# Optimization experiments

Hardware: AMD Instinct MI355X
Metric: run time of the kernel (lower is better)

## Reference

```python
import jax, jax.numpy as jnp
import numpy as np

N_NODES = 100000
N_EDGES = 3200000
# (out_dim, in_dim) for the 4 BayesianLinear layers: mlp1 = [5->16, 16->32], mlp2 = [35->16, 16->1]
LAYER_DIMS = [(16, 5), (32, 16), (16, 35), (1, 16)]


def setup_inputs() -> dict:
    key = jax.random.key(0)
    ks = iter(jax.random.split(key, 32))
    inp = {}
    inp["x"] = jax.random.normal(next(ks), (N_NODES, 3), jnp.float32)
    inp["edge_attr"] = jax.random.normal(next(ks), (N_EDGES, 2), jnp.float32)
    inp["edge_index"] = jax.random.randint(next(ks), (2, N_EDGES), 0, N_NODES, dtype=jnp.int64)
    for li, (o, i) in enumerate(LAYER_DIMS, 1):
        inp[f"l{li}_wmu"] = jax.random.normal(next(ks), (o, i), jnp.float32) * 0.1
        inp[f"l{li}_wrho"] = jax.random.normal(next(ks), (o, i), jnp.float32) * 0.1 - 5.0
        inp[f"l{li}_bmu"] = jax.random.normal(next(ks), (o,), jnp.float32) * 0.1
        inp[f"l{li}_brho"] = jax.random.normal(next(ks), (o,), jnp.float32) * 0.1 - 5.0
        inp[f"l{li}_eps_w"] = jax.random.normal(next(ks), (o, i), jnp.float32)
        inp[f"l{li}_eps_b"] = jax.random.normal(next(ks), (o,), jnp.float32)
    return inp


def _bayes_linear(h, wmu, wrho, bmu, brho, eps_w, eps_b):
    # sampled weight: W = mu + softplus(rho) * eps  (blitz BayesianLinear)
    W = wmu + jax.nn.softplus(wrho) * eps_w          # [out, in]
    b = bmu + jax.nn.softplus(brho) * eps_b          # [out]
    return h @ W.T + b


def _igconv(x, edge_index, edge_attr, p1, p2, p3, p4):
    src, dst = edge_index[0], edge_index[1]          # x_j = x[src], aggregate at dst
    x_j = x[src]                                     # [E, 3] irregular gather
    m = jnp.concatenate([x_j, edge_attr], axis=1)    # [E, 5]
    m = jax.nn.relu(_bayes_linear(m, *p1))           # [E, 16]
    m = jax.nn.relu(_bayes_linear(m, *p2))           # [E, 32]
    agg = jax.ops.segment_max(m, dst, num_segments=x.shape[0])  # [N, 32]
    agg = jnp.where(jnp.isneginf(agg), 0.0, agg)     # nodes with no in-edges -> 0
    h = jnp.concatenate([x, agg], axis=1)            # [N, 35]
    h = jax.nn.relu(_bayes_linear(h, *p3))           # [N, 16]
    comb = jax.nn.sigmoid(_bayes_linear(h, *p4))     # [N, 1]
    return jnp.concatenate([x[:, :2], comb], axis=1) # [N, 3]


def reference(x, edge_attr, edge_index,
              l1_wmu, l1_wrho, l1_bmu, l1_brho, l1_eps_w, l1_eps_b,
              l2_wmu, l2_wrho, l2_bmu, l2_brho, l2_eps_w, l2_eps_b,
              l3_wmu, l3_wrho, l3_bmu, l3_brho, l3_eps_w, l3_eps_b,
              l4_wmu, l4_wrho, l4_bmu, l4_brho, l4_eps_w, l4_eps_b):
    p1 = (l1_wmu, l1_wrho, l1_bmu, l1_brho, l1_eps_w, l1_eps_b)
    p2 = (l2_wmu, l2_wrho, l2_bmu, l2_brho, l2_eps_w, l2_eps_b)
    p3 = (l3_wmu, l3_wrho, l3_bmu, l3_brho, l3_eps_w, l3_eps_b)
    p4 = (l4_wmu, l4_wrho, l4_bmu, l4_brho, l4_eps_w, l4_eps_b)
    h = x
    for _ in range(3):  # three stacked applications of the same IGConv
        h = _igconv(h, edge_index, edge_attr, p1, p2, p3, p4)
    return h
```

## Files before the change

kernel.cpp:

```cpp
#include <hip/hip_runtime.h>
#include <math.h>

#define WTOT  1233
#define PKOFS 1280
#define PKTOT 352

typedef __fp16 h2 __attribute__((ext_vector_type(2)));
typedef __fp16 f16x8 __attribute__((ext_vector_type(8)));
typedef float f32x4 __attribute__((ext_vector_type(4)));

struct ERec { int s; int d; unsigned int ea; };

__device__ __forceinline__ h2 u2h(unsigned int u) { return __builtin_bit_cast(h2, u); }
__device__ __forceinline__ unsigned int h2u(h2 h) { return __builtin_bit_cast(unsigned int, h); }
__device__ __forceinline__ unsigned int umax2(unsigned int a, unsigned int b) {
  return h2u(__builtin_elementwise_max(u2h(a), u2h(b)));
}
#define DOT2(a, b, c) __builtin_amdgcn_fdot2((a), (b), (c), false)

__device__ __forceinline__ float softplus_f(float x) {
  return fmaxf(x, 0.f) + log1pf(expf(-fabsf(x)));
}

struct PrepArgs {
  const float* wmu[4]; const float* wrho[4]; const float* epsw[4];
  const float* bmu[4]; const float* brho[4]; const float* epsb[4];
  float* out;
};

__global__ void prep_all_kernel(PrepArgs a) {
  const int wsz[4] = {80, 512, 560, 16};
  const int wof[4] = {0, 96, 640, 1216};
  const int bsz[4] = {16, 32, 16, 1};
  const int bof[4] = {80, 608, 1200, 1232};
  float* wg = a.out;
  int tid = threadIdx.x;
#pragma unroll
  for (int l = 0; l < 4; l++) {
    for (int i = tid; i < wsz[l]; i += 1024)
      wg[wof[l] + i] = a.wmu[l][i] + softplus_f(a.wrho[l][i]) * a.epsw[l][i];
    for (int i = tid; i < bsz[l]; i += 1024)
      wg[bof[l] + i] = a.bmu[l][i] + softplus_f(a.brho[l][i]) * a.epsb[l][i];
  }
  __syncthreads();
  unsigned int* wp = (unsigned int*)(wg + PKOFS);
  int t = tid;
  if (t < 16) {
    wp[t]      = h2u(h2{(__fp16)wg[t * 5 + 0], (__fp16)wg[t * 5 + 1]});
    wp[16 + t] = h2u(h2{(__fp16)wg[t * 5 + 2], (__fp16)0.f});
    wp[32 + t] = h2u(h2{(__fp16)wg[t * 5 + 3], (__fp16)wg[t * 5 + 4]});
    ((float*)wp)[304 + t] = wg[80 + t];
  }
  if (t < 32) {
    ((float*)wp)[320 + t] = wg[608 + t];
    for (int j = 0; j < 8; j++)
      wp[48 + t * 8 + j] =
          h2u(h2{(__fp16)wg[96 + t * 16 + 2 * j], (__fp16)wg[96 + t * 16 + 2 * j + 1]});
  }
}

__global__ void zero_kernel(int* __restrict__ p, int n) {
  int i = blockIdx.x * blockDim.x + threadIdx.x;
  if (i < n) p[i] = 0;
}

__global__ __launch_bounds__(1024) void bhist_kernel(const int* __restrict__ dst,
                                                     int* __restrict__ bucketCur,
                                                     int E, int NBUCK) {
  __shared__ int h[1024];
  int tid = threadIdx.x;
  for (int i = tid; i < NBUCK; i += 1024) h[i] = 0;
  __syncthreads();
  int base = blockIdx.x * 8192;
#pragma unroll
  for (int r = 0; r < 8; r++) {
    int e = base + r * 1024 + tid;
    if (e < E) atomicAdd(&h[dst[e] >> 7], 1);
  }
  __syncthreads();
  for (int i = tid; i < NBUCK; i += 1024) {
    int c = h[i];
    if (c) atomicAdd(&bucketCur[i], c);
  }
}

__global__ __launch_bounds__(1024) void scanBk_kernel(int* __restrict__ bucketCur,
                                                      int* __restrict__ bucketOff,
                                                      int NBUCK) {
  __shared__ int wsum[16];
  __shared__ int woff[16];
  int tid = threadIdx.x, lane = tid & 63, wid = tid >> 6;
  int v = (tid < NBUCK) ? bucketCur[tid] : 0;
  int x = v;
#pragma unroll
  for (int off = 1; off < 64; off <<= 1) {
    int t = __shfl_up(x, off, 64);
    if (lane >= off) x += t;
  }
  if (lane == 63) wsum[wid] = x;
  __syncthreads();
  if (wid == 0) {
    int s = (lane < 16) ? wsum[lane] : 0;
#pragma unroll
    for (int off = 1; off < 16; off <<= 1) {
      int t = __shfl_up(s, off, 64);
      if (lane >= off) s += t;
    }
    if (lane < 16) woff[lane] = s - wsum[lane];
  }
  __syncthreads();
  int excl = woff[wid] + x - v;
  if (tid < NBUCK) {
    bucketOff[tid] = excl;
    bucketCur[tid] = excl;
    if (tid == NBUCK - 1) bucketOff[NBUCK] = excl + v;
  }
}

__global__ __launch_bounds__(1024) void part_kernel(
    const int* __restrict__ src, const int* __restrict__ dst,
    const float2* __restrict__ ea, int* __restrict__ bucketCur,
    ERec* __restrict__ brec, int E, int NBUCK) {
  __shared__ int h[1024];
  int tid = threadIdx.x;
  for (int i = tid; i < NBUCK; i += 1024) h[i] = 0;
  __syncthreads();
  int base = blockIdx.x * 8192;
  int d[8], s[8];
  unsigned int a[8];
  bool v[8];
#pragma unroll
  for (int j = 0; j < 8; j++) {
    int e = base + j * 1024 + tid;
    v[j] = e < E;
    if (v[j]) {
      d[j] = dst[e];
      s[j] = src[e];
      float2 t = ea[e];
      a[j] = h2u(__builtin_amdgcn_cvt_pkrtz(t.x, t.y));
      atomicAdd(&h[d[j] >> 7], 1);
    }
  }
  __syncthreads();
  for (int i = tid; i < NBUCK; i += 1024) {
    int c = h[i];
    h[i] = c ? atomicAdd(&bucketCur[i], c) : 0;
  }
  __syncthreads();
#pragma unroll
  for (int j = 0; j < 8; j++) {
    if (v[j]) {
      int pos = atomicAdd(&h[d[j] >> 7], 1);
      ERec t; t.s = s[j]; t.d = d[j]; t.ea = a[j];
      brec[pos] = t;
    }
  }
}

__global__ __launch_bounds__(256) void deg_kernel(const ERec* __restrict__ brec,
                                                  const int* __restrict__ bucketOff,
                                                  int* __restrict__ deg, int N) {
  __shared__ int cnt[128];
  int b = blockIdx.x, tid = threadIdx.x;
  if (tid < 128) cnt[tid] = 0;
  __syncthreads();
  int e0 = bucketOff[b], e1 = bucketOff[b + 1];
  for (int i = e0 + tid; i < e1; i += 256) atomicAdd(&cnt[brec[i].d & 127], 1);
  __syncthreads();
  int node = b * 128 + tid;
  if (tid < 128 && node < N) deg[node] = cnt[tid];
}

__global__ void scanA_kernel(const int* __restrict__ deg, int* __restrict__ part, int n) {
  __shared__ int ws[16];
  int tid = threadIdx.x;
  int i = blockIdx.x * 1024 + tid;
  int v = 0;
  if (i < n) v = (deg[i] + 3) & ~3;
#pragma unroll
  for (int off = 32; off >= 1; off >>= 1) v += __shfl_down(v, off, 64);
  if ((tid & 63) == 0) ws[tid >> 6] = v;
  __syncthreads();
  if (tid == 0) {
    int s = 0;
#pragma unroll
    for (int k = 0; k < 16; k++) s += ws[k];
    part[blockIdx.x] = s;
  }
}

__global__ void scanB_kernel(int* __restrict__ part, int P, int* __restrict__ etot) {
  int lane = threadIdx.x;
  int carry = 0;
  for (int base = 0; base < P; base += 64) {
    int i = base + lane;
    int v = (i < P) ? part[i] : 0;
    int x = v;
#pragma unroll
    for (int off = 1; off < 64; off <<= 1) {
      int t = __shfl_up(x, off, 64);
      if (lane >= off) x += t;
    }
    if (i < P) part[i] = carry + x - v;
    carry += __shfl(x, 63, 64);
  }
  if (lane == 0) *etot = carry;
}

__global__ void scanC_kernel(const int* __restrict__ deg, const int* __restrict__ part,
                             int* __restrict__ cursor, int n) {
  __shared__ int wsum[16];
  __shared__ int woff[16];
  int tid = threadIdx.x, lane = tid & 63, wid = tid >> 6;
  int i = blockIdx.x * 1024 + tid;
  int v = 0;
  if (i < n) v = (deg[i] + 3) & ~3;
  int x = v;
#pragma unroll
  for (int off = 1; off < 64; off <<= 1) {
    int t = __shfl_up(x, off, 64);
    if (lane >= off) x += t;
  }
  if (lane == 63) wsum[wid] = x;
  __syncthreads();
  if (wid == 0) {
    int s = (lane < 16) ? wsum[lane] : 0;
#pragma unroll
    for (int off = 1; off < 16; off <<= 1) {
      int t = __shfl_up(s, off, 64);
      if (lane >= off) s += t;
    }
    if (lane < 16) woff[lane] = s - wsum[lane];
  }
  __syncthreads();
  if (i < n) cursor[i] = part[blockIdx.x] + woff[wid] + x - v;
}

__global__ __launch_bounds__(256) void scat_kernel(
    const ERec* __restrict__ brec, const int* __restrict__ bucketOff,
    const int* __restrict__ cursor, ERec* __restrict__ erec, int N) {
  __shared__ int lcur[128];
  int b = blockIdx.x, tid = threadIdx.x;
  int node = b * 128 + tid;
  if (tid < 128) lcur[tid] = (node < N) ? cursor[node] : 0;
  __syncthreads();
  int e0 = bucketOff[b], e1 = bucketOff[b + 1];
  for (int i = e0 + tid; i < e1; i += 256) {
    ERec t = brec[i];
    int pos = atomicAdd(&lcur[t.d & 127], 1);
    erec[pos] = t;
  }
  __syncthreads();
  if (tid < 128 && node < N) {
    int cur = cursor[node];
    int endR = lcur[tid];
    int endP = cur + ((endR - cur + 3) & ~3);
    if (endR > cur) {
      ERec rep = erec[cur];
      for (int k = endR; k < endP; k++) erec[k] = rep;
    }
  }
}

__global__ void xpack_kernel(const float* __restrict__ x, uint2* __restrict__ xpk, int n) {
  int i = blockIdx.x * blockDim.x + threadIdx.x;
  if (i < n) {
    h2 a = __builtin_amdgcn_cvt_pkrtz(x[3 * i], x[3 * i + 1]);
    h2 b = __builtin_amdgcn_cvt_pkrtz(x[3 * i + 2], 0.f);
    xpk[i] = make_uint2(h2u(a), h2u(b));
  }
}

__global__ __launch_bounds__(256) void edge_kernel(
    const uint2* __restrict__ xpk, const ERec* __restrict__ erec,
    unsigned int* __restrict__ agg,
    int* __restrict__ pdstL, unsigned int* __restrict__ pvalL,
    int* __restrict__ pdstR, unsigned int* __restrict__ pvalR,
    const float* __restrict__ wg, const int* __restrict__ pEtot, int N) {
  __shared__ __align__(16) unsigned int lds[4][64][12];
  const unsigned int* wp = (const unsigned int*)(wg + PKOFS);
  const float* bf = (const float*)wp;
  const int Etot = *pEtot;
  const int tid = threadIdx.x;
  const int lane = tid & 63;
  const int wslot = tid >> 6;
  const int e = blockIdx.x * 256 + tid;
  const int wbase = e - lane;
  const int w = wbase >> 6;

  bool vld = e < Etot;
  ERec r;
  r.s = 0; r.d = N; r.ea = 0u;
  if (vld) r = erec[e];
  int d = r.d;
  uint2 xs = xpk[r.s];

  h2 p01 = u2h(xs.x), p2v = u2h(xs.y), pea = u2h(r.ea);
  unsigned int m1[8];
#pragma unroll
  for (int p = 0; p < 8; p++) {
    const int oA = 2 * p, oB = 2 * p + 1;
    float sA = DOT2(p01, u2h(wp[oA]),
                DOT2(p2v, u2h(wp[16 + oA]),
                DOT2(pea, u2h(wp[32 + oA]), bf[304 + oA])));
    float sB = DOT2(p01, u2h(wp[oB]),
                DOT2(p2v, u2h(wp[16 + oB]),
                DOT2(pea, u2h(wp[32 + oB]), bf[304 + oB])));
    m1[p] = h2u(__builtin_amdgcn_cvt_pkrtz(fmaxf(sA, 0.f), fmaxf(sB, 0.f)));
  }

  uint4* rowp = (uint4*)&lds[wslot][lane][0];
  rowp[0] = make_uint4(m1[0], m1[1], m1[2], m1[3]);
  rowp[1] = make_uint4(m1[4], m1[5], m1[6], m1[7]);
  __syncthreads();

  const int fl = lane & 15;
  const int hq = lane >> 4;
  f16x8 bLo = __builtin_bit_cast(f16x8, make_uint4(0u, 0u, 0u, 0u));
  f16x8 bHi = bLo;
  if (hq < 2) {
    bLo = __builtin_bit_cast(f16x8, *(const uint4*)&wp[48 + fl * 8 + 4 * hq]);
    bHi = __builtin_bit_cast(f16x8, *(const uint4*)&wp[48 + (fl + 16) * 8 + 4 * hq]);
  }
  float b2lo = bf[320 + fl], b2hi = bf[336 + fl];

  f32x4 accL[4], accH[4];
#pragma unroll
  for (int g = 0; g < 4; g++) {
    f16x8 afrag = __builtin_bit_cast(f16x8, make_uint4(0u, 0u, 0u, 0u));
    if (hq < 2)
      afrag = __builtin_bit_cast(f16x8, *(const uint4*)&lds[wslot][16 * g + fl][4 * hq]);
    f32x4 cl = {b2lo, b2lo, b2lo, b2lo};
    f32x4 ch = {b2hi, b2hi, b2hi, b2hi};
    accL[g] = __builtin_amdgcn_mfma_f32_16x16x32_f16(afrag, bLo, cl, 0, 0, 0);
    accH[g] = __builtin_amdgcn_mfma_f32_16x16x32_f16(afrag, bHi, ch, 0, 0, 0);
  }

  float bmL[4], bmH[4];
#pragma unroll
  for (int g = 0; g < 4; g++) {
    bmL[g] = fmaxf(fmaxf(accL[g].x, accL[g].y), fmaxf(accL[g].z, fmaxf(accL[g].w, 0.f)));
    bmH[g] = fmaxf(fmaxf(accH[g].x, accH[g].y), fmaxf(accH[g].z, fmaxf(accH[g].w, 0.f)));
  }

  int dprev = __shfl_up(d, 1, 64);
  bool isHead = (lane == 0) || (d != dprev);
  unsigned long long hm = __ballot(isHead);
  int dp = -2, dn = -2;
  if (lane == 0 && wbase > 0) dp = erec[wbase - 1].d;
  if (lane == 63 && wbase + 64 < Etot) dn = erec[wbase + 64].d;
  dp = __shfl(dp, 0, 64);
  dn = __shfl(dn, 63, 64);

  unsigned long long rem = hm;
  while (rem) {
    int a = (int)__builtin_ctzll(rem);
    rem &= rem - 1;
    int b = rem ? (int)__builtin_ctzll(rem) : 64;
    int rd = __shfl(d, a, 64);
    int A = a >> 2, B = b >> 2;
    float mlo = 0.f, mhi = 0.f;
#pragma unroll
    for (int g = 0; g < 4; g++) {
      int blk = 4 * g + hq;
      bool in = (blk >= A) && (blk < B);
      mlo = fmaxf(mlo, in ? bmL[g] : 0.f);
      mhi = fmaxf(mhi, in ? bmH[g] : 0.f);
    }
    mlo = fmaxf(mlo, __shfl_xor(mlo, 16, 64));
    mlo = fmaxf(mlo, __shfl_xor(mlo, 32, 64));
    mhi = fmaxf(mhi, __shfl_xor(mhi, 16, 64));
    mhi = fmaxf(mhi, __shfl_xor(mhi, 32, 64));
    unsigned int pkv = h2u(__builtin_amdgcn_cvt_pkrtz(mlo, mhi));
    bool contL = (a == 0) && (rd == dp);
    bool contR = (b == 64) && (rd == dn);
    if (!contL && !contR) {
      if (lane < 16) agg[(size_t)rd * 16 + fl] = pkv;
    } else if (contL) {
      if (lane < 16) {
        if (lane == 0) pdstL[w] = rd;
        pvalL[w * 16 + fl] = pkv;
      }
    } else {
      if (lane < 16) {
        if (lane == 0) pdstR[w] = rd;
        pvalR[w * 16 + fl] = pkv;
      }
    }
  }
}

__device__ __forceinline__ void max4(uint4& a, uint4 b) {
  a.x = umax2(a.x, b.x); a.y = umax2(a.y, b.y);
  a.z = umax2(a.z, b.z); a.w = umax2(a.w, b.w);
}

__global__ __launch_bounds__(256) void node_kernel(
    const float* __restrict__ x, const float* __restrict__ cin,
    float* __restrict__ cout, uint2* __restrict__ xpk,
    float* __restrict__ outFinal, const unsigned int* __restrict__ agg,
    const int* __restrict__ deg, const int* __restrict__ cursor,
    const int* __restrict__ pdstL, const uint4* __restrict__ pvalL,
    const int* __restrict__ pdstR, const uint4* __restrict__ pvalR,
    const float* __restrict__ wg, int n) {
  int nid = blockIdx.x * blockDim.x + threadIdx.x;
  if (nid >= n) return;
  int dg = deg[nid];
  uint4 q0 = make_uint4(0u, 0u, 0u, 0u), q1 = q0, q2 = q0, q3 = q0;
  if (dg > 0) {
    int r0 = cursor[nid];
    int r1 = r0 + dg;
    int w0 = r0 >> 6, w1 = (r1 - 1) >> 6;
    if (w0 == w1) {
      const uint4* a = (const uint4*)(agg + (size_t)nid * 16);
      q0 = a[0]; q1 = a[1]; q2 = a[2]; q3 = a[3];
    } else {
      if (pdstR[w0] == nid) {
        q0 = pvalR[w0 * 4 + 0]; q1 = pvalR[w0 * 4 + 1];
        q2 = pvalR[w0 * 4 + 2]; q3 = pvalR[w0 * 4 + 3];
      }
      for (int w = w0 + 1; w <= w1; w++) {
        if (pdstL[w] == nid) {
          max4(q0, pvalL[w * 4 + 0]); max4(q1, pvalL[w * 4 + 1]);
          max4(q2, pvalL[w * 4 + 2]); max4(q3, pvalL[w * 4 + 3]);
        }
      }
    }
  }
  unsigned int pkv[16] = {q0.x, q0.y, q0.z, q0.w, q1.x, q1.y, q1.z, q1.w,
                          q2.x, q2.y, q2.z, q2.w, q3.x, q3.y, q3.z, q3.w};
  float av[32];
#pragma unroll
  for (int i = 0; i < 16; i++) {
    h2 h = u2h(pkv[i]);
    av[i] = (float)h.x;
    av[16 + i] = (float)h.y;
  }
  float x0 = x[3 * nid], x1 = x[3 * nid + 1];
  float x2 = cin ? cin[nid] : x[3 * nid + 2];
  float h[16];
#pragma unroll
  for (int o = 0; o < 16; o++) {
    float sa = wg[1200 + o];
    sa = fmaf(wg[640 + o * 35 + 0], x0, sa);
    sa = fmaf(wg[640 + o * 35 + 1], x1, sa);
    sa = fmaf(wg[640 + o * 35 + 2], x2, sa);
#pragma unroll
    for (int k = 0; k < 32; k++) sa = fmaf(wg[640 + o * 35 + 3 + k], av[k], sa);
    h[o] = fmaxf(sa, 0.f);
  }
  float z = wg[1232];
#pragma unroll
  for (int k = 0; k < 16; k++) z = fmaf(wg[1216 + k], h[k], z);
  float comb = 1.f / (1.f + expf(-z));
  cout[nid] = comb;
  ((unsigned int*)xpk)[2 * nid + 1] = h2u(__builtin_amdgcn_cvt_pkrtz(comb, 0.f));
  if (outFinal) {
    outFinal[3 * nid] = x0;
    outFinal[3 * nid + 1] = x1;
    outFinal[3 * nid + 2] = comb;
  }
}

extern "C" void kernel_launch(void* const* d_in, const int* in_sizes, int n_in,
                              void* d_out, int out_size, void* d_ws, size_t ws_size,
                              hipStream_t stream) {
  const float* x = (const float*)d_in[0];
  const float* ea = (const float*)d_in[1];
  const int* eidx = (const int*)d_in[2];
  const int N = in_sizes[0] / 3;
  const int E = in_sizes[1] / 2;
  const int* src = eidx;
  const int* dst = eidx + E;
  const int P = (N + 1023) / 1024;
  const int NBUCK = (N + 127) >> 7;
  const int EP = E + 3 * N;
  const int NWP = (EP + 63) / 64;

  char* p = (char*)d_ws;
  size_t off = 0;
  auto alloc = [&](size_t bytes) -> char* {
    char* r = p + off;
    off = (off + bytes + 255) & ~(size_t)255;
    return r;
  };
  float* wbuf = (float*)alloc((size_t)(PKOFS + PKTOT) * 4);
  int* deg = (int*)alloc((size_t)N * 4);
  int* part = (int*)alloc((size_t)P * 4);
  int* cursor = (int*)alloc((size_t)N * 4);
  int* bucketOff = (int*)alloc(((size_t)NBUCK + 1) * 4);
  int* bucketCur = (int*)alloc((size_t)NBUCK * 4);
  int* etot = (int*)alloc(4);
  ERec* erec = (ERec*)alloc((size_t)EP * sizeof(ERec));
  char* uni = alloc((size_t)E * 12);
  ERec* brec = (ERec*)uni;
  size_t uoff = 0;
  auto ualloc = [&](size_t bytes) -> char* {
    char* r = uni + uoff;
    uoff = (uoff + bytes + 255) & ~(size_t)255;
    return r;
  };
  unsigned int* agg = (unsigned int*)ualloc(((size_t)N + 1) * 16 * 4);
  uint2* xpk = (uint2*)ualloc((size_t)N * 8);
  int* pdstL = (int*)ualloc((size_t)NWP * 4);
  int* pdstR = (int*)ualloc((size_t)NWP * 4);
  unsigned int* pvalL = (unsigned int*)ualloc((size_t)NWP * 64);
  unsigned int* pvalR = (unsigned int*)ualloc((size_t)NWP * 64);
  float* bufA = (float*)ualloc((size_t)N * 4);
  float* bufB = (float*)ualloc((size_t)N * 4);
  (void)ws_size;

  PrepArgs pa;
  for (int l = 0; l < 4; l++) {
    pa.wmu[l] = (const float*)d_in[3 + 6 * l + 0];
    pa.wrho[l] = (const float*)d_in[3 + 6 * l + 1];
    pa.bmu[l] = (const float*)d_in[3 + 6 * l + 2];
    pa.brho[l] = (const float*)d_in[3 + 6 * l + 3];
    pa.epsw[l] = (const float*)d_in[3 + 6 * l + 4];
    pa.epsb[l] = (const float*)d_in[3 + 6 * l + 5];
  }
  pa.out = wbuf;

  const int TB = 256;
  auto blocks = [&](int n) { return dim3((n + TB - 1) / TB); };

  prep_all_kernel<<<dim3(1), dim3(1024), 0, stream>>>(pa);
  zero_kernel<<<blocks(NBUCK), dim3(TB), 0, stream>>>(bucketCur, NBUCK);
  bhist_kernel<<<dim3((E + 8191) / 8192), dim3(1024), 0, stream>>>(dst, bucketCur, E, NBUCK);
  scanBk_kernel<<<dim3(1), dim3(1024), 0, stream>>>(bucketCur, bucketOff, NBUCK);
  part_kernel<<<dim3((E + 8191) / 8192), dim3(1024), 0, stream>>>(
      src, dst, (const float2*)ea, bucketCur, brec, E, NBUCK);
  deg_kernel<<<dim3(NBUCK), dim3(TB), 0, stream>>>(brec, bucketOff, deg, N);
  scanA_kernel<<<dim3(P), dim3(1024), 0, stream>>>(deg, part, N);
  scanB_kernel<<<dim3(1), dim3(64), 0, stream>>>(part, P, etot);
  scanC_kernel<<<dim3(P), dim3(1024), 0, stream>>>(deg, part, cursor, N);
  scat_kernel<<<dim3(NBUCK), dim3(TB), 0, stream>>>(brec, bucketOff, cursor, erec, N);
  xpack_kernel<<<blocks(N), dim3(TB), 0, stream>>>(x, xpk, N);

  float* outp = (float*)d_out;
  const int ebp = (EP + 255) / 256;
  edge_kernel<<<dim3(ebp), dim3(TB), 0, stream>>>(xpk, erec, agg, pdstL, pvalL, pdstR,
                                                  pvalR, wbuf, etot, N);
  node_kernel<<<blocks(N), dim3(TB), 0, stream>>>(x, nullptr, bufA, xpk, nullptr, agg,
                                                  deg, cursor, pdstL, (const uint4*)pvalL,
                                                  pdstR, (const uint4*)pvalR, wbuf, N);
  edge_kernel<<<dim3(ebp), dim3(TB), 0, stream>>>(xpk, erec, agg, pdstL, pvalL, pdstR,
                                                  pvalR, wbuf, etot, N);
  node_kernel<<<blocks(N), dim3(TB), 0, stream>>>(x, bufA, bufB, xpk, nullptr, agg,
                                                  deg, cursor, pdstL, (const uint4*)pvalL,
                                                  pdstR, (const uint4*)pvalR, wbuf, N);
  edge_kernel<<<dim3(ebp), dim3(TB), 0, stream>>>(xpk, erec, agg, pdstL, pvalL, pdstR,
                                                  pvalR, wbuf, etot, N);
  node_kernel<<<blocks(N), dim3(TB), 0, stream>>>(x, bufB, bufA, xpk, outp, agg,
                                                  deg, cursor, pdstL, (const uint4*)pvalL,
                                                  pdstR, (const uint4*)pvalR, wbuf, N);
}
```

Before: 389.8 us.

## Replace boundary-partial aggregation with fp32 atomicMax and use 32x32 MFMA

Segment-max results are now written with global atomicMax on fp32 bit patterns into a 32-float-per-node buffer. Non-negative floats order the same as their unsigned bits, so no separate boundary-partial arrays (pdstL/pvalL/pdstR/pvalR) or node-side merge over wavefront boundaries are needed. The node kernel reads the aggregate and zeroes it for the next layer, and xpack does the first zeroing. The second edge layer switches from eight 16x16x32 MFMAs to two 32x32x16 MFMAs, with heads taken at 4-edge granularity. Other changes: bucket zeroing is folded into the prep kernel, part_kernel handles 16K edges per block and reloads edge data instead of keeping it in registers, and edge blocks past the edge count exit early. The trade-off is atomic traffic, and agg storage doubles from fp16 pairs to fp32.

```diff
diff --git a/kernel.cpp b/kernel.cpp
--- a/kernel.cpp
+++ b/kernel.cpp
@@ -7,15 +7,12 @@
 
 typedef __fp16 h2 __attribute__((ext_vector_type(2)));
 typedef __fp16 f16x8 __attribute__((ext_vector_type(8)));
-typedef float f32x4 __attribute__((ext_vector_type(4)));
+typedef float f32x16 __attribute__((ext_vector_type(16)));
 
 struct ERec { int s; int d; unsigned int ea; };
 
 __device__ __forceinline__ h2 u2h(unsigned int u) { return __builtin_bit_cast(h2, u); }
 __device__ __forceinline__ unsigned int h2u(h2 h) { return __builtin_bit_cast(unsigned int, h); }
-__device__ __forceinline__ unsigned int umax2(unsigned int a, unsigned int b) {
-  return h2u(__builtin_elementwise_max(u2h(a), u2h(b)));
-}
 #define DOT2(a, b, c) __builtin_amdgcn_fdot2((a), (b), (c), false)
 
 __device__ __forceinline__ float softplus_f(float x) {
@@ -25,7 +22,7 @@
 struct PrepArgs {
   const float* wmu[4]; const float* wrho[4]; const float* epsw[4];
   const float* bmu[4]; const float* brho[4]; const float* epsb[4];
-  float* out;
+  float* out; int* bucketCur; int nbuck;
 };
 
 __global__ void prep_all_kernel(PrepArgs a) {
@@ -35,6 +32,7 @@
   const int bof[4] = {80, 608, 1200, 1232};
   float* wg = a.out;
   int tid = threadIdx.x;
+  if (tid < a.nbuck) a.bucketCur[tid] = 0;
 #pragma unroll
   for (int l = 0; l < 4; l++) {
     for (int i = tid; i < wsz[l]; i += 1024)
@@ -57,11 +55,6 @@
       wp[48 + t * 8 + j] =
           h2u(h2{(__fp16)wg[96 + t * 16 + 2 * j], (__fp16)wg[96 + t * 16 + 2 * j + 1]});
   }
-}
-
-__global__ void zero_kernel(int* __restrict__ p, int n) {
-  int i = blockIdx.x * blockDim.x + threadIdx.x;
-  if (i < n) p[i] = 0;
 }
 
 __global__ __launch_bounds__(1024) void bhist_kernel(const int* __restrict__ dst,
@@ -125,21 +118,11 @@
   int tid = threadIdx.x;
   for (int i = tid; i < NBUCK; i += 1024) h[i] = 0;
   __syncthreads();
-  int base = blockIdx.x * 8192;
-  int d[8], s[8];
-  unsigned int a[8];
-  bool v[8];
-#pragma unroll
-  for (int j = 0; j < 8; j++) {
+  int base = blockIdx.x * 16384;
+#pragma unroll
+  for (int j = 0; j < 16; j++) {
     int e = base + j * 1024 + tid;
-    v[j] = e < E;
-    if (v[j]) {
-      d[j] = dst[e];
-      s[j] = src[e];
-      float2 t = ea[e];
-      a[j] = h2u(__builtin_amdgcn_cvt_pkrtz(t.x, t.y));
-      atomicAdd(&h[d[j] >> 7], 1);
-    }
+    if (e < E) atomicAdd(&h[dst[e] >> 7], 1);
   }
   __syncthreads();
   for (int i = tid; i < NBUCK; i += 1024) {
@@ -148,11 +131,17 @@
   }
   __syncthreads();
 #pragma unroll
-  for (int j = 0; j < 8; j++) {
-    if (v[j]) {
-      int pos = atomicAdd(&h[d[j] >> 7], 1);
-      ERec t; t.s = s[j]; t.d = d[j]; t.ea = a[j];
-      brec[pos] = t;
+  for (int j = 0; j < 16; j++) {
+    int e = base + j * 1024 + tid;
+    if (e < E) {
+      int dd = dst[e];
+      float2 t = ea[e];
+      ERec rec;
+      rec.s = src[e];
+      rec.d = dd;
+      rec.ea = h2u(__builtin_amdgcn_cvt_pkrtz(t.x, t.y));
+      int pos = atomicAdd(&h[dd >> 7], 1);
+      brec[pos] = rec;
     }
   }
 }
@@ -262,31 +251,38 @@
   }
 }
 
-__global__ void xpack_kernel(const float* __restrict__ x, uint2* __restrict__ xpk, int n) {
+__global__ void xpack_kernel(const float* __restrict__ x, uint2* __restrict__ xpk,
+                             unsigned int* __restrict__ agg32, int n) {
   int i = blockIdx.x * blockDim.x + threadIdx.x;
   if (i < n) {
     h2 a = __builtin_amdgcn_cvt_pkrtz(x[3 * i], x[3 * i + 1]);
     h2 b = __builtin_amdgcn_cvt_pkrtz(x[3 * i + 2], 0.f);
     xpk[i] = make_uint2(h2u(a), h2u(b));
+    uint4 z = make_uint4(0u, 0u, 0u, 0u);
+    uint4* ap = (uint4*)(agg32 + (size_t)i * 32);
+#pragma unroll
+    for (int k = 0; k < 8; k++) ap[k] = z;
+    if (i == 0) {
+      uint4* as = (uint4*)(agg32 + (size_t)n * 32);
+#pragma unroll
+      for (int k = 0; k < 8; k++) as[k] = z;
+    }
   }
 }
 
 __global__ __launch_bounds__(256) void edge_kernel(
     const uint2* __restrict__ xpk, const ERec* __restrict__ erec,
-    unsigned int* __restrict__ agg,
-    int* __restrict__ pdstL, unsigned int* __restrict__ pvalL,
-    int* __restrict__ pdstR, unsigned int* __restrict__ pvalR,
+    unsigned int* __restrict__ agg32,
     const float* __restrict__ wg, const int* __restrict__ pEtot, int N) {
   __shared__ __align__(16) unsigned int lds[4][64][12];
   const unsigned int* wp = (const unsigned int*)(wg + PKOFS);
   const float* bf = (const float*)wp;
   const int Etot = *pEtot;
+  if (blockIdx.x * 256 >= Etot) return;
   const int tid = threadIdx.x;
   const int lane = tid & 63;
   const int wslot = tid >> 6;
   const int e = blockIdx.x * 256 + tid;
-  const int wbase = e - lane;
-  const int w = wbase >> 6;
 
   bool vld = e < Etot;
   ERec r;
@@ -312,45 +308,34 @@
   uint4* rowp = (uint4*)&lds[wslot][lane][0];
   rowp[0] = make_uint4(m1[0], m1[1], m1[2], m1[3]);
   rowp[1] = make_uint4(m1[4], m1[5], m1[6], m1[7]);
-  __syncthreads();
-
-  const int fl = lane & 15;
-  const int hq = lane >> 4;
-  f16x8 bLo = __builtin_bit_cast(f16x8, make_uint4(0u, 0u, 0u, 0u));
-  f16x8 bHi = bLo;
-  if (hq < 2) {
-    bLo = __builtin_bit_cast(f16x8, *(const uint4*)&wp[48 + fl * 8 + 4 * hq]);
-    bHi = __builtin_bit_cast(f16x8, *(const uint4*)&wp[48 + (fl + 16) * 8 + 4 * hq]);
-  }
-  float b2lo = bf[320 + fl], b2hi = bf[336 + fl];
-
-  f32x4 accL[4], accH[4];
-#pragma unroll
-  for (int g = 0; g < 4; g++) {
-    f16x8 afrag = __builtin_bit_cast(f16x8, make_uint4(0u, 0u, 0u, 0u));
-    if (hq < 2)
-      afrag = __builtin_bit_cast(f16x8, *(const uint4*)&lds[wslot][16 * g + fl][4 * hq]);
-    f32x4 cl = {b2lo, b2lo, b2lo, b2lo};
-    f32x4 ch = {b2hi, b2hi, b2hi, b2hi};
-    accL[g] = __builtin_amdgcn_mfma_f32_16x16x32_f16(afrag, bLo, cl, 0, 0, 0);
-    accH[g] = __builtin_amdgcn_mfma_f32_16x16x32_f16(afrag, bHi, ch, 0, 0, 0);
-  }
-
-  float bmL[4], bmH[4];
-#pragma unroll
-  for (int g = 0; g < 4; g++) {
-    bmL[g] = fmaxf(fmaxf(accL[g].x, accL[g].y), fmaxf(accL[g].z, fmaxf(accL[g].w, 0.f)));
-    bmH[g] = fmaxf(fmaxf(accH[g].x, accH[g].y), fmaxf(accH[g].z, fmaxf(accH[g].w, 0.f)));
-  }
-
-  int dprev = __shfl_up(d, 1, 64);
-  bool isHead = (lane == 0) || (d != dprev);
+  asm volatile("s_waitcnt lgkmcnt(0)" ::: "memory");
+  __builtin_amdgcn_sched_barrier(0);
+
+  const int col = lane & 31;
+  const int h = lane >> 5;
+  f16x8 bfrag = __builtin_bit_cast(f16x8, *(const uint4*)&wp[48 + col * 8 + 4 * h]);
+  float bias = bf[320 + col];
+  f32x16 cini;
+#pragma unroll
+  for (int i = 0; i < 16; i++) cini[i] = bias;
+
+  f16x8 a0 = __builtin_bit_cast(f16x8, *(const uint4*)&lds[wslot][col][4 * h]);
+  f16x8 a1 = __builtin_bit_cast(f16x8, *(const uint4*)&lds[wslot][32 + col][4 * h]);
+  f32x16 acc0 = __builtin_amdgcn_mfma_f32_32x32x16_f16(a0, bfrag, cini, 0, 0, 0);
+  f32x16 acc1 = __builtin_amdgcn_mfma_f32_32x32x16_f16(a1, bfrag, cini, 0, 0, 0);
+
+  float bm[2][4];
+#pragma unroll
+  for (int q = 0; q < 4; q++) {
+    bm[0][q] = fmaxf(fmaxf(acc0[4 * q], acc0[4 * q + 1]),
+                     fmaxf(acc0[4 * q + 2], fmaxf(acc0[4 * q + 3], 0.f)));
+    bm[1][q] = fmaxf(fmaxf(acc1[4 * q], acc1[4 * q + 1]),
+                     fmaxf(acc1[4 * q + 2], fmaxf(acc1[4 * q + 3], 0.f)));
+  }
+
+  int dp4 = __shfl_up(d, 4, 64);
+  bool isHead = ((lane & 3) == 0) && (lane == 0 || d != dp4);
   unsigned long long hm = __ballot(isHead);
-  int dp = -2, dn = -2;
-  if (lane == 0 && wbase > 0) dp = erec[wbase - 1].d;
-  if (lane == 63 && wbase + 64 < Etot) dn = erec[wbase + 64].d;
-  dp = __shfl(dp, 0, 64);
-  dn = __shfl(dn, 63, 64);
 
   unsigned long long rem = hm;
   while (rem) {
@@ -359,82 +344,43 @@
     int b = rem ? (int)__builtin_ctzll(rem) : 64;
     int rd = __shfl(d, a, 64);
     int A = a >> 2, B = b >> 2;
-    float mlo = 0.f, mhi = 0.f;
-#pragma unroll
-    for (int g = 0; g < 4; g++) {
-      int blk = 4 * g + hq;
-      bool in = (blk >= A) && (blk < B);
-      mlo = fmaxf(mlo, in ? bmL[g] : 0.f);
-      mhi = fmaxf(mhi, in ? bmH[g] : 0.f);
-    }
-    mlo = fmaxf(mlo, __shfl_xor(mlo, 16, 64));
-    mlo = fmaxf(mlo, __shfl_xor(mlo, 32, 64));
-    mhi = fmaxf(mhi, __shfl_xor(mhi, 16, 64));
-    mhi = fmaxf(mhi, __shfl_xor(mhi, 32, 64));
-    unsigned int pkv = h2u(__builtin_amdgcn_cvt_pkrtz(mlo, mhi));
-    bool contL = (a == 0) && (rd == dp);
-    bool contR = (b == 64) && (rd == dn);
-    if (!contL && !contR) {
-      if (lane < 16) agg[(size_t)rd * 16 + fl] = pkv;
-    } else if (contL) {
-      if (lane < 16) {
-        if (lane == 0) pdstL[w] = rd;
-        pvalL[w * 16 + fl] = pkv;
+    float mx = 0.f;
+#pragma unroll
+    for (int g = 0; g < 2; g++) {
+#pragma unroll
+      for (int q = 0; q < 4; q++) {
+        int blk = 8 * g + 2 * q + h;
+        bool in = (blk >= A) && (blk < B);
+        mx = fmaxf(mx, in ? bm[g][q] : 0.f);
       }
-    } else {
-      if (lane < 16) {
-        if (lane == 0) pdstR[w] = rd;
-        pvalR[w * 16 + fl] = pkv;
-      }
-    }
-  }
-}
-
-__device__ __forceinline__ void max4(uint4& a, uint4 b) {
-  a.x = umax2(a.x, b.x); a.y = umax2(a.y, b.y);
-  a.z = umax2(a.z, b.z); a.w = umax2(a.w, b.w);
+    }
+    mx = fmaxf(mx, __shfl_xor(mx, 32, 64));
+    if (lane < 32 && rd < N)
+      atomicMax(agg32 + (size_t)rd * 32 + col, __float_as_uint(mx));
+  }
 }
 
 __global__ __launch_bounds__(256) void node_kernel(
     const float* __restrict__ x, const float* __restrict__ cin,
     float* __restrict__ cout, uint2* __restrict__ xpk,
-    float* __restrict__ outFinal, const unsigned int* __restrict__ agg,
-    const int* __restrict__ deg, const int* __restrict__ cursor,
-    const int* __restrict__ pdstL, const uint4* __restrict__ pvalL,
-    const int* __restrict__ pdstR, const uint4* __restrict__ pvalR,
+    float* __restrict__ outFinal, unsigned int* __restrict__ agg32,
     const float* __restrict__ wg, int n) {
   int nid = blockIdx.x * blockDim.x + threadIdx.x;
   if (nid >= n) return;
-  int dg = deg[nid];
-  uint4 q0 = make_uint4(0u, 0u, 0u, 0u), q1 = q0, q2 = q0, q3 = q0;
-  if (dg > 0) {
-    int r0 = cursor[nid];
-    int r1 = r0 + dg;
-    int w0 = r0 >> 6, w1 = (r1 - 1) >> 6;
-    if (w0 == w1) {
-      const uint4* a = (const uint4*)(agg + (size_t)nid * 16);
-      q0 = a[0]; q1 = a[1]; q2 = a[2]; q3 = a[3];
-    } else {
-      if (pdstR[w0] == nid) {
-        q0 = pvalR[w0 * 4 + 0]; q1 = pvalR[w0 * 4 + 1];
-        q2 = pvalR[w0 * 4 + 2]; q3 = pvalR[w0 * 4 + 3];
-      }
-      for (int w = w0 + 1; w <= w1; w++) {
-        if (pdstL[w] == nid) {
-          max4(q0, pvalL[w * 4 + 0]); max4(q1, pvalL[w * 4 + 1]);
-          max4(q2, pvalL[w * 4 + 2]); max4(q3, pvalL[w * 4 + 3]);
-        }
-      }
-    }
-  }
-  unsigned int pkv[16] = {q0.x, q0.y, q0.z, q0.w, q1.x, q1.y, q1.z, q1.w,
-                          q2.x, q2.y, q2.z, q2.w, q3.x, q3.y, q3.z, q3.w};
+  uint4* ap = (uint4*)(agg32 + (size_t)nid * 32);
+  uint4 q[8];
+#pragma unroll
+  for (int i = 0; i < 8; i++) q[i] = ap[i];
+  uint4 z = make_uint4(0u, 0u, 0u, 0u);
+#pragma unroll
+  for (int i = 0; i < 8; i++) ap[i] = z;
   float av[32];
 #pragma unroll
-  for (int i = 0; i < 16; i++) {
-    h2 h = u2h(pkv[i]);
-    av[i] = (float)h.x;
-    av[16 + i] = (float)h.y;
+  for (int i = 0; i < 8; i++) {
+    av[4 * i + 0] = __uint_as_float(q[i].x);
+    av[4 * i + 1] = __uint_as_float(q[i].y);
+    av[4 * i + 2] = __uint_as_float(q[i].z);
+    av[4 * i + 3] = __uint_as_float(q[i].w);
   }
   float x0 = x[3 * nid], x1 = x[3 * nid + 1];
   float x2 = cin ? cin[nid] : x[3 * nid + 2];
@@ -449,10 +395,10 @@
     for (int k = 0; k < 32; k++) sa = fmaf(wg[640 + o * 35 + 3 + k], av[k], sa);
     h[o] = fmaxf(sa, 0.f);
   }
-  float z = wg[1232];
-#pragma unroll
-  for (int k = 0; k < 16; k++) z = fmaf(wg[1216 + k], h[k], z);
-  float comb = 1.f / (1.f + expf(-z));
+  float z4 = wg[1232];
+#pragma unroll
+  for (int k = 0; k < 16; k++) z4 = fmaf(wg[1216 + k], h[k], z4);
+  float comb = 1.f / (1.f + expf(-z4));
   cout[nid] = comb;
   ((unsigned int*)xpk)[2 * nid + 1] = h2u(__builtin_amdgcn_cvt_pkrtz(comb, 0.f));
   if (outFinal) {
@@ -475,7 +421,6 @@
   const int P = (N + 1023) / 1024;
   const int NBUCK = (N + 127) >> 7;
   const int EP = E + 3 * N;
-  const int NWP = (EP + 63) / 64;
 
   char* p = (char*)d_ws;
   size_t off = 0;
@@ -500,12 +445,8 @@
     uoff = (uoff + bytes + 255) & ~(size_t)255;
     return r;
   };
-  unsigned int* agg = (unsigned int*)ualloc(((size_t)N + 1) * 16 * 4);
+  unsigned int* agg32 = (unsigned int*)ualloc(((size_t)N + 1) * 32 * 4);
   uint2* xpk = (uint2*)ualloc((size_t)N * 8);
-  int* pdstL = (int*)ualloc((size_t)NWP * 4);
-  int* pdstR = (int*)ualloc((size_t)NWP * 4);
-  unsigned int* pvalL = (unsigned int*)ualloc((size_t)NWP * 64);
-  unsigned int* pvalR = (unsigned int*)ualloc((size_t)NWP * 64);
   float* bufA = (float*)ualloc((size_t)N * 4);
   float* bufB = (float*)ualloc((size_t)N * 4);
   (void)ws_size;
@@ -520,38 +461,33 @@
     pa.epsb[l] = (const float*)d_in[3 + 6 * l + 5];
   }
   pa.out = wbuf;
+  pa.bucketCur = bucketCur;
+  pa.nbuck = NBUCK;
 
   const int TB = 256;
   auto blocks = [&](int n) { return dim3((n + TB - 1) / TB); };
 
   prep_all_kernel<<<dim3(1), dim3(1024), 0, stream>>>(pa);
-  zero_kernel<<<blocks(NBUCK), dim3(TB), 0, stream>>>(bucketCur, NBUCK);
   bhist_kernel<<<dim3((E + 8191) / 8192), dim3(1024), 0, stream>>>(dst, bucketCur, E, NBUCK);
   scanBk_kernel<<<dim3(1), dim3(1024), 0, stream>>>(bucketCur, bucketOff, NBUCK);
-  part_kernel<<<dim3((E + 8191) / 8192), dim3(1024), 0, stream>>>(
+  part_kernel<<<dim3((E + 16383) / 16384), dim3(1024), 0, stream>>>(
       src, dst, (const float2*)ea, bucketCur, brec, E, NBUCK);
   deg_kernel<<<dim3(NBUCK), dim3(TB), 0, stream>>>(brec, bucketOff, deg, N);
   scanA_kernel<<<dim3(P), dim3(1024), 0, stream>>>(deg, part, N);
   scanB_kernel<<<dim3(1), dim3(64), 0, stream>>>(part, P, etot);
   scanC_kernel<<<dim3(P), dim3(1024), 0, stream>>>(deg, part, cursor, N);
   scat_kernel<<<dim3(NBUCK), dim3(TB), 0, stream>>>(brec, bucketOff, cursor, erec, N);
-  xpack_kernel<<<blocks(N), dim3(TB), 0, stream>>>(x, xpk, N);
+  xpack_kernel<<<blocks(N), dim3(TB), 0, stream>>>(x, xpk, agg32, N);
 
   float* outp = (float*)d_out;
   const int ebp = (EP + 255) / 256;
-  edge_kernel<<<dim3(ebp), dim3(TB), 0, stream>>>(xpk, erec, agg, pdstL, pvalL, pdstR,
-                                                  pvalR, wbuf, etot, N);
-  node_kernel<<<blocks(N), dim3(TB), 0, stream>>>(x, nullptr, bufA, xpk, nullptr, agg,
-                                                  deg, cursor, pdstL, (const uint4*)pvalL,
-                                                  pdstR, (const uint4*)pvalR, wbuf, N);
-  edge_kernel<<<dim3(ebp), dim3(TB), 0, stream>>>(xpk, erec, agg, pdstL, pvalL, pdstR,
-                                                  pvalR, wbuf, etot, N);
-  node_kernel<<<blocks(N), dim3(TB), 0, stream>>>(x, bufA, bufB, xpk, nullptr, agg,
-                                                  deg, cursor, pdstL, (const uint4*)pvalL,
-                                                  pdstR, (const uint4*)pvalR, wbuf, N);
-  edge_kernel<<<dim3(ebp), dim3(TB), 0, stream>>>(xpk, erec, agg, pdstL, pvalL, pdstR,
-                                                  pvalR, wbuf, etot, N);
-  node_kernel<<<blocks(N), dim3(TB), 0, stream>>>(x, bufB, bufA, xpk, outp, agg,
-                                                  deg, cursor, pdstL, (const uint4*)pvalL,
-                                                  pdstR, (const uint4*)pvalR, wbuf, N);
-}
+  edge_kernel<<<dim3(ebp), dim3(TB), 0, stream>>>(xpk, erec, agg32, wbuf, etot, N);
+  node_kernel<<<blocks(N), dim3(TB), 0, stream>>>(x, nullptr, bufA, xpk, nullptr,
+                                                  agg32, wbuf, N);
+  edge_kernel<<<dim3(ebp), dim3(TB), 0, stream>>>(xpk, erec, agg32, wbuf, etot, N);
+  node_kernel<<<blocks(N), dim3(TB), 0, stream>>>(x, bufA, bufB, xpk, nullptr,
+                                                  agg32, wbuf, N);
+  edge_kernel<<<dim3(ebp), dim3(TB), 0, stream>>>(xpk, erec, agg32, wbuf, etot, N);
+  node_kernel<<<blocks(N), dim3(TB), 0, stream>>>(x, bufB, bufA, xpk, outp,
+                                                  agg32, wbuf, N);
+}
```

Result: slower. 423.3 us (+8.6%).
